# Optimization experiments

Hardware: AMD Instinct MI355X
Metric: run time of the kernel (lower is better)

The kernel has to match this reference:

```python
import jax, jax.numpy as jnp
import numpy as np

VOCAB = 41      # len(MOL_DICT) + 1
EMB = 512       # EMBEDDING_SIZE
HID = 1024
B, T = 128, 256


def setup_inputs() -> dict:
    key = jax.random.key(0)
    ks = jax.random.split(key, 8)
    x = jax.random.randint(ks[0], (B, T), 0, VOCAB)
    # realistic prefix padding mask: True for valid tokens, False for padding
    lengths = jax.random.randint(ks[1], (B,), T // 4, T + 1)
    padding_mask = jnp.arange(T)[None, :] < lengths[:, None]
    s = 0.05
    emb_table = jax.random.normal(ks[2], (VOCAB, EMB), jnp.float32) * s
    gru_kernel = jax.random.normal(ks[3], (EMB, 3 * HID), jnp.float32) * s
    gru_rec_kernel = jax.random.normal(ks[4], (HID, 3 * HID), jnp.float32) * s
    gru_bias = jax.random.normal(ks[5], (2, 3 * HID), jnp.float32) * s
    dense_w = jax.random.normal(ks[6], (HID, VOCAB), jnp.float32) * s
    dense_b = jnp.zeros((VOCAB,), jnp.float32)
    return {"x": x, "padding_mask": padding_mask, "emb_table": emb_table,
            "gru_kernel": gru_kernel, "gru_rec_kernel": gru_rec_kernel,
            "gru_bias": gru_bias, "dense_w": dense_w, "dense_b": dense_b}


def _gru_scan(x_proj_t, mask_t, rec_kernel, rec_bias):
    # x_proj_t: [T, B, 3H] precomputed input projections; mask_t: [T, B] bool
    def step(h, inp):
        xp, m = inp                      # xp: [B, 3H], m: [B]
        rec = h @ rec_kernel + rec_bias  # [B, 3H]  (reset_after=True)
        xz, xr, xh = jnp.split(xp, 3, axis=-1)
        rz, rr, rh = jnp.split(rec, 3, axis=-1)
        z = jax.nn.sigmoid(xz + rz)
        r = jax.nn.sigmoid(xr + rr)
        hh = jnp.tanh(xh + r * rh)
        h_new = z * h + (1.0 - z) * hh
        # masked steps carry previous state/output forward (keras semantics)
        h = jnp.where(m[:, None], h_new, h)
        return h, h

    h0 = jnp.zeros((x_proj_t.shape[1], HID), x_proj_t.dtype)
    _, outs = jax.lax.scan(step, h0, (x_proj_t, mask_t))
    return outs  # [T, B, H]


def reference(x, padding_mask, emb_table, gru_kernel, gru_rec_kernel,
              gru_bias, dense_w, dense_b):
    xe = emb_table[x]                              # [B, T, E]
    x_proj = xe @ gru_kernel + gru_bias[0]         # [B, T, 3H]
    outs = _gru_scan(jnp.transpose(x_proj, (1, 0, 2)),
                     jnp.transpose(padding_mask, (1, 0)),
                     gru_rec_kernel, gru_bias[1])  # [T, B, H]
    h = jnp.transpose(outs, (1, 0, 2))             # [B, T, H]
    logits = h @ dense_w + dense_b                 # [B, T, VOCAB]
    return logits
```

## Files before the change

kernel.cpp:

```cpp
#include <hip/hip_runtime.h>
#include <stdint.h>
#include <stddef.h>

#define VOCAB 41
#define EMB   512
#define HID   1024
#define H3    3072
#define BB    128
#define TT    256
#define BT    (BB*TT)
#define NSLOT 4
#define SLOT_U32 (8*32*512)

typedef unsigned short u16;
typedef uint32_t u32;
typedef _Float16 half_t;
typedef half_t f16x8 __attribute__((ext_vector_type(8)));
typedef float f32x4 __attribute__((ext_vector_type(4)));
typedef u32 u32x4 __attribute__((ext_vector_type(4)));

__device__ __forceinline__ float bf2f(u16 u) {
  return __uint_as_float(((uint32_t)u) << 16);
}
__device__ __forceinline__ u16 f2bf(float f) {
  uint32_t x = __float_as_uint(f);
  return (u16)((x + 0x7FFFu + ((x >> 16) & 1u)) >> 16);
}
__device__ __forceinline__ u16 f2h_bits(float f) {
  half_t h = (half_t)f;
  return __builtin_bit_cast(u16, h);
}
__device__ __forceinline__ float sigmoidf_(float x) {
  return 1.0f / (1.0f + __expf(-x));
}
__device__ __forceinline__ float tanh_fast(float x) {
  return 1.0f - 2.0f / (__expf(2.0f * x) + 1.0f);
}


__global__ void detect_kernel(const u16* __restrict__ raw, int* __restrict__ flag) {
  __shared__ int s[256];
  int tid = threadIdx.x, cnt = 0;
  for (int i = tid; i < 4096; i += 256) {
    int e = (raw[i] >> 7) & 0xFF;
    if (e >= 132) cnt++;
  }
  s[tid] = cnt; __syncthreads();
  if (tid == 0) {
    int tot = 0;
    for (int i = 0; i < 256; i++) tot += s[i];
    *flag = (tot > 4) ? 1 : 0;
  }
}

__global__ void conv_kernel(const void* __restrict__ src, float* __restrict__ dst,
                            int n, const int* __restrict__ flag) {
  int i = blockIdx.x * 256 + threadIdx.x;
  if (i >= n) return;
  if (*flag) dst[i] = ((const float*)src)[i];
  else       dst[i] = bf2f(((const u16*)src)[i]);
}

__global__ void tokm_kernel(const int* __restrict__ x,
                            const unsigned char* __restrict__ m,
                            int* __restrict__ tokm) {
  int i = blockIdx.x * 256 + threadIdx.x;
  unsigned char b0 = m[0], b1 = m[1];
  bool t;
  if (b0 == 1) {
    if (b1 != 0) t = (m[i] != 0);
    else         t = (((const int*)m)[i] != 0);
  } else if (b0 == 0x80) {
    t = (((const u16*)m)[i] != 0);
  } else {
    t = (((const float*)m)[i] != 0.0f);
  }
  tokm[i] = x[i] | (t ? 0 : 0x80000000);
}

__global__ __launch_bounds__(256) void proj_kernel(
    const void* __restrict__ emb, const void* __restrict__ gk,
    const float* __restrict__ gbf, float* __restrict__ P,
    const int* __restrict__ flag) {
  int v = blockIdx.x / (H3 / 256);
  int j = (blockIdx.x % (H3 / 256)) * 256 + threadIdx.x;
  float acc = gbf[j];
  if (*flag) {
    const float* e = (const float*)emb + v * EMB;
    const float* g = (const float*)gk;
    for (int k = 0; k < EMB; ++k) acc = fmaf(e[k], g[k * H3 + j], acc);
  } else {
    const u16* e = (const u16*)emb + v * EMB;
    const u16* g = (const u16*)gk;
    for (int k = 0; k < EMB; ++k) acc = fmaf(bf2f(e[k]), bf2f(g[k * H3 + j]), acc);
  }
  P[v * H3 + j] = acc;
}

__global__ void p2_kernel(const float* __restrict__ P, const float* __restrict__ gbf,
                          float* __restrict__ P2) {
  int gc = blockIdx.x;
  int v = threadIdx.x;
  if (v >= VOCAB) return;
  float val = P[v * H3 + gc];
  if (gc < 2048) val += gbf[H3 + gc];
  P2[gc * VOCAB + v] = val;
}

__global__ void pack_wimg_kernel(const void* __restrict__ src, u16* __restrict__ img,
                                 const int* __restrict__ flag) {
  int idx = blockIdx.x * 256 + threadIdx.x;
  int j = idx & 7;
  int t1 = idx >> 3;
  int lane = t1 & 63;
  int t2 = t1 >> 6;
  int c = t2 % 6;
  int t3 = t2 / 6;
  int ks = t3 & 31;
  int ds = t3 >> 5;
  int g = c >> 1, dh = c & 1;
  int k = ks * 32 + (lane >> 4) * 8 + j;
  int col = g * 1024 + ds * 32 + dh * 16 + (lane & 15);
  float val;
  if (*flag) val = ((const float*)src)[(size_t)k * H3 + col];
  else       val = bf2f(((const u16*)src)[(size_t)k * H3 + col]);
  img[idx] = f2h_bits(val);
}

__global__ void pack_dimg_kernel(const void* __restrict__ src, u16* __restrict__ img,
                                 const int* __restrict__ flag) {
  int idx = blockIdx.x * 256 + threadIdx.x;
  int j = idx & 7;
  int t1 = idx >> 3;
  int lane = t1 & 63;
  int t2 = t1 >> 6;
  int ct = t2 % 3;
  int ks = t2 / 3;
  int k = ks * 32 + (lane >> 4) * 8 + j;
  int v = ct * 16 + (lane & 15);
  float val = 0.0f;
  if (v < VOCAB) {
    if (*flag) val = ((const float*)src)[(size_t)k * VOCAB + v];
    else       val = bf2f(((const u16*)src)[(size_t)k * VOCAB + v]);
  }
  img[idx] = f2h_bits(val);
}

__global__ __launch_bounds__(256, 1) void gru_persist(
    const uint4* __restrict__ Wimg, const int* __restrict__ tokm,
    const float* __restrict__ P2, const float* __restrict__ gbf,
    u32* __restrict__ exch, u16* __restrict__ Hout) {
  int bid = blockIdx.x;
  int gt = bid & 7, ds = bid >> 3;
  int tid = threadIdx.x;
  int w = tid >> 6, lane = tid & 63;

  __shared__ float red[4][64][25];
  __shared__ __align__(16) u16 tr[512];
  __shared__ float Pl[3][32][41];
  __shared__ int tokL[16 * 259];

  f16x8 breg[6][8];
  {
    const uint4* wsrc = Wimg + (size_t)ds * (32 * 6) * 64 + lane;
    #pragma unroll
    for (int k8 = 0; k8 < 8; ++k8)
      #pragma unroll
      for (int c = 0; c < 6; ++c)
        breg[c][k8] = __builtin_bit_cast(f16x8, wsrc[((w * 8 + k8) * 6 + c) * 64]);
  }

  for (int i = tid; i < 3 * 32 * VOCAB; i += 256) {
    int v = i % VOCAB;
    int t1 = i / VOCAB;
    int di = t1 & 31, g = t1 >> 5;
    Pl[g][di][v] = P2[(size_t)(g * 1024 + ds * 32 + di) * VOCAB + v];
  }
  for (int i = tid; i < 16 * 256; i += 256) {
    int rr = i >> 8, cc = i & 255;
    tokL[rr * 259 + cc] = tokm[gt * 4096 + i];
  }

  int row = tid >> 4, dimb = tid & 15;
  int lane_src = (row >> 2) * 16 + dimb;
  int rg = row & 3;
  float b1h0 = gbf[H3 + 2048 + ds * 32 + dimb];
  float b1h1 = gbf[H3 + 2048 + ds * 32 + dimb + 16];
  float hc0 = 0.f, hc1 = 0.f;
  __syncthreads();

  u32x4 d[16];
  for (int t = 0; t < TT; ++t) {
    const u32* slotb = exch + (size_t)(t & (NSLOT - 1)) * SLOT_U32;
    {
      const u32* sp = slotb + (size_t)(gt * 32 + (w * 8 + (lane & 7))) * 512 + 511;
      int cap = 0;
      while (true) {
        u32 v = __hip_atomic_load(sp, __ATOMIC_RELAXED, __HIP_MEMORY_SCOPE_AGENT);
        if (__ballot((v >> 16) != (u32)t) == 0ULL) break;
        __builtin_amdgcn_s_sleep(1);
        if (++cap > (1 << 16)) break;
      }
    }
    {
      const u32* abase = slotb + (size_t)(gt * 32 + w * 8) * 512 + lane * 8;
      int cap = 0;
      while (true) {
        #pragma unroll
        for (int i = 0; i < 8; ++i) {
          asm volatile("global_load_dwordx4 %0, %2, off sc1\n\t"
                       "global_load_dwordx4 %1, %2, off offset:16 sc1"
                       : "=&v"(d[2 * i]), "=&v"(d[2 * i + 1])
                       : "v"(abase + (size_t)i * 512) : "memory");
        }
        asm volatile("s_waitcnt vmcnt(0)" ::: "memory");
        __builtin_amdgcn_sched_barrier(0);
        u32 want = ((u32)t) << 16, bad = 0;
        #pragma unroll
        for (int i = 0; i < 16; ++i) {
          u32x4 q = d[i];
          bad |= (q.x ^ want) | (q.y ^ want) | (q.z ^ want) | (q.w ^ want);
        }
        bad &= 0xFFFF0000u;
        if (__ballot(bad != 0) == 0ULL) break;
        __builtin_amdgcn_s_sleep(1);
        if (++cap > (1 << 16)) break;
      }
    }

    f32x4 acc[6];
    #pragma unroll
    for (int c = 0; c < 6; ++c) acc[c] = (f32x4){0.f, 0.f, 0.f, 0.f};
    #pragma unroll
    for (int k8 = 0; k8 < 8; ++k8) {
      u32x4 lo = d[2 * k8], hi = d[2 * k8 + 1];
      u32x4 pk;
      pk.x = (lo.y << 16) | (lo.x & 0xFFFFu);
      pk.y = (lo.w << 16) | (lo.z & 0xFFFFu);
      pk.z = (hi.y << 16) | (hi.x & 0xFFFFu);
      pk.w = (hi.w << 16) | (hi.z & 0xFFFFu);
      f16x8 a = __builtin_bit_cast(f16x8, pk);
      #pragma unroll
      for (int c = 0; c < 6; ++c)
        acc[c] = __builtin_amdgcn_mfma_f32_16x16x32_f16(a, breg[c][k8], acc[c], 0, 0, 0);
    }

    {
      float* q = red[w][lane];
      #pragma unroll
      for (int c = 0; c < 6; ++c)
        #pragma unroll
        for (int r = 0; r < 4; ++r) q[c * 4 + r] = acc[c][r];
    }
    __syncthreads();

    {
      int tm = tokL[row * 259 + t];
      int tok = tm & 0xFFFF;
      #pragma unroll
      for (int dh = 0; dh < 2; ++dh) {
        float a0 = 0.f, a1 = 0.f, a2 = 0.f;
        #pragma unroll
        for (int ww = 0; ww < 4; ++ww) {
          const float* q = red[ww][lane_src];
          a0 += q[(0 * 2 + dh) * 4 + rg];
          a1 += q[(1 * 2 + dh) * 4 + rg];
          a2 += q[(2 * 2 + dh) * 4 + rg];
        }
        int dglob = dimb + dh * 16;
        float z  = sigmoidf_(Pl[0][dglob][tok] + a0);
        float r_ = sigmoidf_(Pl[1][dglob][tok] + a1);
        float b1h = dh ? b1h1 : b1h0;
        float hh = tanh_fast(Pl[2][dglob][tok] + r_ * (a2 + b1h));
        float h = dh ? hc1 : hc0;
        if (tm >= 0) h = z * h + (1.0f - z) * hh;
        if (dh) hc1 = h; else hc0 = h;
        tr[(dglob >> 3) * 128 + row * 8 + (dglob & 7)] = f2h_bits(h);
      }
    }
    __syncthreads();

    if (w == 0) {
      u32x4 tr4 = ((const u32x4*)tr)[lane];
      u32 tag1 = ((u32)(t + 1)) << 16;
      u32x4 o0, o1;
      o0.x = tag1 | (tr4.x & 0xFFFFu); o0.y = tag1 | (tr4.x >> 16);
      o0.z = tag1 | (tr4.y & 0xFFFFu); o0.w = tag1 | (tr4.y >> 16);
      o1.x = tag1 | (tr4.z & 0xFFFFu); o1.y = tag1 | (tr4.z >> 16);
      o1.z = tag1 | (tr4.w & 0xFFFFu); o1.w = tag1 | (tr4.w >> 16);
      u32* eb = exch + (size_t)((t + 1) & (NSLOT - 1)) * SLOT_U32 +
                (size_t)(gt * 32 + ds) * 512 + lane * 8;
      asm volatile("global_store_dwordx4 %0, %1, off sc1\n\t"
                   "global_store_dwordx4 %0, %2, off offset:16 sc1"
                   :: "v"(eb), "v"(o0), "v"(o1) : "memory");
      {
        int quad = lane >> 4, mm = lane & 15;
        int b = gt * 16 + mm;
        size_t idx = ((size_t)(b * 16 + (t >> 4)) * 32 + ds) * 64 +
                     quad * 16 + (t & 15);
        ((u32x4*)Hout)[idx] = tr4;
      }
    }
  }
}

__global__ __launch_bounds__(256) void dense_mfma(
    const u16* __restrict__ HoutImg, const uint4* __restrict__ dimg,
    const float* __restrict__ dbf, void* __restrict__ out,
    const int* __restrict__ flag) {
  __shared__ uint4 Bl[48 * 64];
  int tid = threadIdx.x;
  int w = tid >> 6, lane = tid & 63;
  int quad = lane >> 4, vi = lane & 15;
  int gt0 = blockIdx.x * 8 + w * 2;

  f32x4 acc[2][3];
  #pragma unroll
  for (int i = 0; i < 2; ++i)
    #pragma unroll
    for (int c = 0; c < 3; ++c) acc[i][c] = (f32x4){0.f, 0.f, 0.f, 0.f};

  for (int half = 0; half < 2; ++half) {
    for (int i = tid; i < 48 * 64; i += 256) Bl[i] = dimg[half * 48 * 64 + i];
    __syncthreads();
    #pragma unroll
    for (int ks16 = 0; ks16 < 16; ++ks16) {
      int ks = half * 16 + ks16;
      f16x8 a0 = __builtin_bit_cast(
          f16x8, ((const uint4*)HoutImg)[((size_t)gt0 * 32 + ks) * 64 + lane]);
      f16x8 a1 = __builtin_bit_cast(
          f16x8, ((const uint4*)HoutImg)[(((size_t)gt0 + 1) * 32 + ks) * 64 + lane]);
      #pragma unroll
      for (int c = 0; c < 3; ++c) {
        f16x8 bf = __builtin_bit_cast(f16x8, Bl[(ks16 * 3 + c) * 64 + lane]);
        acc[0][c] = __builtin_amdgcn_mfma_f32_16x16x32_f16(a0, bf, acc[0][c], 0, 0, 0);
        acc[1][c] = __builtin_amdgcn_mfma_f32_16x16x32_f16(a1, bf, acc[1][c], 0, 0, 0);
      }
    }
    __syncthreads();
  }

  int isf = *flag;
  #pragma unroll
  for (int i = 0; i < 2; ++i) {
    #pragma unroll
    for (int c = 0; c < 3; ++c) {
      int v = c * 16 + vi;
      if (v >= VOCAB) continue;
      float bias = dbf[v];
      #pragma unroll
      for (int rg = 0; rg < 4; ++rg) {
        size_t bt = (size_t)(gt0 + i) * 16 + quad * 4 + rg;
        float val = acc[i][c][rg] + bias;
        if (isf) ((float*)out)[bt * VOCAB + v] = val;
        else     ((u16*)out)[bt * VOCAB + v] = f2bf(val);
      }
    }
  }
}


extern "C" void kernel_launch(void* const* d_in, const int* in_sizes, int n_in,
                              void* d_out, int out_size, void* d_ws, size_t ws_size,
                              hipStream_t stream) {
  const int* x            = (const int*)d_in[0];
  const unsigned char* mk = (const unsigned char*)d_in[1];

  char* ws = (char*)d_ws;
  int*   flag  = (int*)(ws + 0);
  float* dbf   = (float*)(ws + 4 * 1024);
  float* gbf   = (float*)(ws + 8 * 1024);
  int*   tokm  = (int*)(ws + 64 * 1024);
  u16*   dimg  = (u16*)(ws + 192 * 1024);
  float* P     = (float*)(ws + 288 * 1024);
  float* P2    = (float*)(ws + 800 * 1024);
  u32*   exch  = (u32*)(ws + 1312 * 1024);
  u16*   Wimg  = (u16*)(ws + 3456 * 1024);
  u16*   Hout  = (u16*)(ws + 10 * 1024 * 1024);

  detect_kernel<<<1, 256, 0, stream>>>((const u16*)d_in[4], flag);
  conv_kernel<<<(2 * H3 + 255) / 256, 256, 0, stream>>>(d_in[5], gbf, 2 * H3, flag);
  conv_kernel<<<1, 256, 0, stream>>>(d_in[7], dbf, VOCAB, flag);
  tokm_kernel<<<BT / 256, 256, 0, stream>>>(x, mk, tokm);
  proj_kernel<<<VOCAB * (H3 / 256), 256, 0, stream>>>(d_in[2], d_in[3], gbf, P, flag);
  p2_kernel<<<H3, 64, 0, stream>>>(P, gbf, P2);
  pack_wimg_kernel<<<(32 * 32 * 6 * 64 * 8) / 256, 256, 0, stream>>>(d_in[4], Wimg, flag);
  pack_dimg_kernel<<<(32 * 3 * 64 * 8) / 256, 256, 0, stream>>>(d_in[6], dimg, flag);
  hipMemsetAsync(exch, 0, (size_t)NSLOT * SLOT_U32 * 4, stream);

  gru_persist<<<256, 256, 0, stream>>>((const uint4*)Wimg, tokm, P2, gbf,
                                       exch, Hout);
  dense_mfma<<<256, 256, 0, stream>>>(Hout, (const uint4*)dimg, dbf, d_out, flag);
}
```

Before: 1.153 ms.

## Rework GRU cross-block polling with sampled tag probes and cache-coherence fallback

Merges the two-stage wait (a tag-word spin, then a full-vector reload) into one loop. The loop polls 64 tag words spread across each slot, then loads the full slot using sc0 loads instead of sc1. If polling goes on too long it switches to sc0 sc1 (system-coherent) loads as a fallback. The producer now stores each exchange vector twice, once plain and once with sc1, so the data reaches both the local cache and the coherent level. The aim is lower per-step handoff latency in the persistent recurrent loop, at the cost of extra stores and some memory-ordering risk on MI355X.

```diff
diff --git a/kernel.cpp b/kernel.cpp
--- a/kernel.cpp
+++ b/kernel.cpp
@@ -189,33 +189,43 @@
   float hc0 = 0.f, hc1 = 0.f;
   __syncthreads();
 
+  int coh = 0;
   u32x4 d[16];
   for (int t = 0; t < TT; ++t) {
     const u32* slotb = exch + (size_t)(t & (NSLOT - 1)) * SLOT_U32;
-    {
-      const u32* sp = slotb + (size_t)(gt * 32 + (w * 8 + (lane & 7))) * 512 + 511;
-      int cap = 0;
-      while (true) {
-        u32 v = __hip_atomic_load(sp, __ATOMIC_RELAXED, __HIP_MEMORY_SCOPE_AGENT);
-        if (__ballot((v >> 16) != (u32)t) == 0ULL) break;
-        __builtin_amdgcn_s_sleep(1);
-        if (++cap > (1 << 16)) break;
-      }
-    }
-    {
-      const u32* abase = slotb + (size_t)(gt * 32 + w * 8) * 512 + lane * 8;
-      int cap = 0;
-      while (true) {
-        #pragma unroll
-        for (int i = 0; i < 8; ++i) {
-          asm volatile("global_load_dwordx4 %0, %2, off sc1\n\t"
-                       "global_load_dwordx4 %1, %2, off offset:16 sc1"
-                       : "=&v"(d[2 * i]), "=&v"(d[2 * i + 1])
-                       : "v"(abase + (size_t)i * 512) : "memory");
+    const u32* abase = slotb + (size_t)(gt * 32 + w * 8) * 512 + lane * 8;
+    const u32* sp = slotb + (size_t)(gt * 32 + w * 8 + (lane >> 3)) * 512 +
+                    (lane & 7) * 73;
+    u32 want = ((u32)t) << 16;
+    int tries = 0;
+    while (true) {
+      u32 v;
+      if (!coh)
+        asm volatile("global_load_dword %0, %1, off sc0\n\ts_waitcnt vmcnt(0)"
+                     : "=v"(v) : "v"(sp) : "memory");
+      else
+        asm volatile("global_load_dword %0, %1, off sc0 sc1\n\ts_waitcnt vmcnt(0)"
+                     : "=v"(v) : "v"(sp) : "memory");
+      __builtin_amdgcn_sched_barrier(0);
+      if (__ballot((v & 0xFFFF0000u) != want) == 0ULL) {
+        if (!coh) {
+          #pragma unroll
+          for (int i = 0; i < 8; ++i)
+            asm volatile("global_load_dwordx4 %0, %2, off sc0\n\t"
+                         "global_load_dwordx4 %1, %2, off offset:16 sc0"
+                         : "=&v"(d[2 * i]), "=&v"(d[2 * i + 1])
+                         : "v"(abase + (size_t)i * 512) : "memory");
+        } else {
+          #pragma unroll
+          for (int i = 0; i < 8; ++i)
+            asm volatile("global_load_dwordx4 %0, %2, off sc0 sc1\n\t"
+                         "global_load_dwordx4 %1, %2, off offset:16 sc0 sc1"
+                         : "=&v"(d[2 * i]), "=&v"(d[2 * i + 1])
+                         : "v"(abase + (size_t)i * 512) : "memory");
         }
         asm volatile("s_waitcnt vmcnt(0)" ::: "memory");
         __builtin_amdgcn_sched_barrier(0);
-        u32 want = ((u32)t) << 16, bad = 0;
+        u32 bad = 0;
         #pragma unroll
         for (int i = 0; i < 16; ++i) {
           u32x4 q = d[i];
@@ -223,9 +233,10 @@
         }
         bad &= 0xFFFF0000u;
         if (__ballot(bad != 0) == 0ULL) break;
-        __builtin_amdgcn_s_sleep(1);
-        if (++cap > (1 << 16)) break;
       }
+      __builtin_amdgcn_s_sleep(1);
+      if (++tries > 1024) coh = 1;
+      if (tries > (1 << 17)) break;
     }
 
     f32x4 acc[6];
@@ -290,7 +301,9 @@
       o1.z = tag1 | (tr4.w & 0xFFFFu); o1.w = tag1 | (tr4.w >> 16);
       u32* eb = exch + (size_t)((t + 1) & (NSLOT - 1)) * SLOT_U32 +
                 (size_t)(gt * 32 + ds) * 512 + lane * 8;
-      asm volatile("global_store_dwordx4 %0, %1, off sc1\n\t"
+      asm volatile("global_store_dwordx4 %0, %1, off\n\t"
+                   "global_store_dwordx4 %0, %2, off offset:16\n\t"
+                   "global_store_dwordx4 %0, %1, off sc1\n\t"
                    "global_store_dwordx4 %0, %2, off offset:16 sc1"
                    :: "v"(eb), "v"(o0), "v"(o1) : "memory");
       {
```

After: 1.503 ms. 1.3x slower.
